# Performance work log

Hardware: AMD Instinct MI355X
Metric: run time of the kernel (lower is better)

## Reference

```python
import jax, jax.numpy as jnp
import numpy as np

BETA = 0.25       # commit-loss weight (beta)
INIT_GAIN = 0.02  # trunc_normal std for codebook init
B, L, D = 4, 4096, 3
VOCAB = 8192


def setup_inputs() -> dict:
    key = jax.random.key(0)
    k1, k2 = jax.random.split(key)
    feats = jax.random.normal(k1, (B, L, D), dtype=jnp.float32)
    # frozen codebook (nn.Embedding weight), trunc_normal(std=0.02) approximated by normal*0.02
    emb = jax.random.normal(k2, (VOCAB, D), dtype=jnp.float32) * INIT_GAIN
    return {"feats": feats, "emb": emb}


def reference(feats, emb):
    b, l, d = feats.shape
    flat = feats.reshape(-1, d)                                # [N, D]
    dist = (jnp.sum(flat * flat, axis=1, keepdims=True)
            - 2.0 * (flat @ emb.T)
            + jnp.sum(emb * emb, axis=1))
    idx = jnp.argmin(dist, axis=1)                             # [N] int
    quant = emb[idx].reshape(b, l, d)                          # gather lookup
    # e_latent_loss: codebook->encoder MSE (feats detached); commit: beta * encoder->codebook MSE
    e_latent_loss = jnp.mean((quant - jax.lax.stop_gradient(feats)) ** 2)
    commit_loss = BETA * jnp.mean((feats - jax.lax.stop_gradient(quant)) ** 2)
    vq_loss = e_latent_loss + commit_loss
    # straight-through estimator
    quant_ste = feats + jax.lax.stop_gradient(quant - feats)
    return quant_ste, idx.reshape(b, l), vq_loss
```

## Files before the change

kernel.cpp:

```cpp
#include <hip/hip_runtime.h>
#include <cstdint>

#define N_ROWS   16384
#define VOCAB    8192
#define CHUNK    1024
#define BLOCK    256
#define NCHUNK   (VOCAB / CHUNK)
#define NRB      (N_ROWS / BLOCK)


__global__ __launch_bounds__(BLOCK) void vq_dist_kernel(
    const float* __restrict__ feats, const float* __restrict__ emb,
    unsigned long long* __restrict__ keys)
{
    __shared__ float4 sE[CHUNK];

    const int chunk = blockIdx.y;
    const int vbase = chunk * CHUNK;

    for (int i = threadIdx.x; i < CHUNK; i += BLOCK) {
        const int v = vbase + i;
        const float e0 = emb[3 * v + 0];
        const float e1 = emb[3 * v + 1];
        const float e2 = emb[3 * v + 2];
        const float ee = __fadd_rn(__fadd_rn(__fmul_rn(e0, e0), __fmul_rn(e1, e1)),
                                   __fmul_rn(e2, e2));
        sE[i] = make_float4(e0, e1, e2, ee);
    }
    __syncthreads();

    const int row = blockIdx.x * BLOCK + threadIdx.x;
    const float x0 = feats[3 * row + 0];
    const float x1 = feats[3 * row + 1];
    const float x2 = feats[3 * row + 2];
    const float xx = __fadd_rn(__fadd_rn(__fmul_rn(x0, x0), __fmul_rn(x1, x1)),
                               __fmul_rn(x2, x2));

    float best = __int_as_float(0x7f800000);
    int   bidx = 0;

    #pragma unroll 8
    for (int i = 0; i < CHUNK; ++i) {
        const float4 E = sE[i];
        const float xe = __fmaf_rn(x2, E.z, __fmaf_rn(x1, E.y, __fmul_rn(x0, E.x)));
        const float d = __fadd_rn(__fsub_rn(xx, __fmul_rn(2.0f, xe)), E.w);
        if (d < best) { best = d; bidx = i; }
    }

    const unsigned long long key =
        ((unsigned long long)__float_as_uint(best) << 32) |
        (unsigned long long)(unsigned)(vbase + bidx);
    atomicMin(&keys[row], key);
}

__global__ __launch_bounds__(BLOCK) void vq_finalize_kernel(
    const float* __restrict__ feats, const float* __restrict__ emb,
    const unsigned long long* __restrict__ keys,
    float* __restrict__ out_quant, float* __restrict__ out_idx,
    float* __restrict__ partial)
{
    const int row = blockIdx.x * BLOCK + threadIdx.x;
    const unsigned long long key = keys[row];
    const unsigned idx = (unsigned)(key & 0xffffffffULL);

    const float x0 = feats[3 * row + 0];
    const float x1 = feats[3 * row + 1];
    const float x2 = feats[3 * row + 2];
    const float e0 = emb[3 * idx + 0];
    const float e1 = emb[3 * idx + 1];
    const float e2 = emb[3 * idx + 2];

    out_quant[3 * row + 0] = __fadd_rn(x0, __fsub_rn(e0, x0));
    out_quant[3 * row + 1] = __fadd_rn(x1, __fsub_rn(e1, x1));
    out_quant[3 * row + 2] = __fadd_rn(x2, __fsub_rn(e2, x2));
    out_idx[row] = (float)idx;

    const float d0 = e0 - x0, d1 = e1 - x1, d2 = e2 - x2;
    float s = d0 * d0 + d1 * d1 + d2 * d2;

    #pragma unroll
    for (int off = 32; off > 0; off >>= 1) s += __shfl_down(s, off, 64);

    __shared__ float wsum[BLOCK / 64];
    if ((threadIdx.x & 63) == 0) wsum[threadIdx.x >> 6] = s;
    __syncthreads();
    if (threadIdx.x == 0)
        partial[blockIdx.x] = (wsum[0] + wsum[1]) + (wsum[2] + wsum[3]);
}

__global__ void vq_loss_kernel(const float* __restrict__ partial,
                               float* __restrict__ out_loss)
{
    float s = partial[threadIdx.x];
    #pragma unroll
    for (int off = 32; off > 0; off >>= 1) s += __shfl_down(s, off, 64);
    if (threadIdx.x == 0) {
        const float m = s / (float)(N_ROWS * 3);
        out_loss[0] = __fadd_rn(m, __fmul_rn(0.25f, m));
    }
}

extern "C" void kernel_launch(void* const* d_in, const int* in_sizes, int n_in,
                              void* d_out, int out_size, void* d_ws, size_t ws_size,
                              hipStream_t stream)
{
    const float* feats = (const float*)d_in[0];
    const float* emb   = (const float*)d_in[1];
    float* out = (float*)d_out;

    unsigned long long* keys = (unsigned long long*)d_ws;
    float* partial = (float*)((char*)d_ws + (size_t)N_ROWS * 8);

    hipMemsetAsync(d_ws, 0xFF, (size_t)N_ROWS * 8, stream);

    vq_dist_kernel<<<dim3(NRB, NCHUNK), BLOCK, 0, stream>>>(feats, emb, keys);
    vq_finalize_kernel<<<NRB, BLOCK, 0, stream>>>(
        feats, emb, keys, out, out + (size_t)N_ROWS * 3, partial);
    vq_loss_kernel<<<1, 64, 0, stream>>>(partial, out + (size_t)N_ROWS * 4);
}
```

Measured before the change: 90.67 us.

## Fuse distance search and finalize into one kernel with 16 lanes per row

Replaces the chunked distance kernel plus 64-bit global atomicMin with one kernel. Each block handles 32 rows, 16 lanes per row, and streams the whole codebook through shared memory in 8 pieces, prefetching the next piece into registers. The row's argmin is reduced with wave shuffles, and the gather, quantized output and loss partial are written in the same kernel, which removes the memset, the atomics and the separate finalize launch. The cost is that every block now reads the full codebook and synchronises 16 times, and only 1 in 16 lanes does the epilogue work.

```diff
diff --git a/kernel.cpp b/kernel.cpp
--- a/kernel.cpp
+++ b/kernel.cpp
@@ -3,99 +3,113 @@
 
 #define N_ROWS   16384
 #define VOCAB    8192
-#define CHUNK    1024
-#define BLOCK    256
-#define NCHUNK   (VOCAB / CHUNK)
-#define NRB      (N_ROWS / BLOCK)
+#define BLOCK    512
+#define ROWS_PB  32
+#define NPIECE   8
+#define PIECE    1024
+#define GRID     (N_ROWS / ROWS_PB)
+
+typedef unsigned long long u64;
 
 
-__global__ __launch_bounds__(BLOCK) void vq_dist_kernel(
+__global__ __launch_bounds__(BLOCK, 4) void vq_main_kernel(
     const float* __restrict__ feats, const float* __restrict__ emb,
-    unsigned long long* __restrict__ keys)
+    float* __restrict__ out_quant, float* __restrict__ out_idx,
+    float* __restrict__ partial)
 {
-    __shared__ float4 sE[CHUNK];
+    __shared__ float4 sE[PIECE];
+    __shared__ float  wsum[BLOCK / 64];
 
-    const int chunk = blockIdx.y;
-    const int vbase = chunk * CHUNK;
+    const int tid = threadIdx.x;
+    const int c   = tid & 15;
+    const int row = blockIdx.x * ROWS_PB + (tid >> 4);
 
-    for (int i = threadIdx.x; i < CHUNK; i += BLOCK) {
-        const int v = vbase + i;
-        const float e0 = emb[3 * v + 0];
-        const float e1 = emb[3 * v + 1];
-        const float e2 = emb[3 * v + 2];
-        const float ee = __fadd_rn(__fadd_rn(__fmul_rn(e0, e0), __fmul_rn(e1, e1)),
-                                   __fmul_rn(e2, e2));
-        sE[i] = make_float4(e0, e1, e2, ee);
-    }
-    __syncthreads();
-
-    const int row = blockIdx.x * BLOCK + threadIdx.x;
     const float x0 = feats[3 * row + 0];
     const float x1 = feats[3 * row + 1];
     const float x2 = feats[3 * row + 2];
     const float xx = __fadd_rn(__fadd_rn(__fmul_rn(x0, x0), __fmul_rn(x1, x1)),
                                __fmul_rn(x2, x2));
 
+    const float* g = emb + 3 * tid;
+    float a0 = g[0],    a1 = g[1],    a2 = g[2];
+    float b0 = g[1536], b1 = g[1537], b2 = g[1538];
+
     float best = __int_as_float(0x7f800000);
-    int   bidx = 0;
+    int   bj   = 0;
 
-    #pragma unroll 8
-    for (int i = 0; i < CHUNK; ++i) {
-        const float4 E = sE[i];
-        const float xe = __fmaf_rn(x2, E.z, __fmaf_rn(x1, E.y, __fmul_rn(x0, E.x)));
-        const float d = __fadd_rn(__fsub_rn(xx, __fmul_rn(2.0f, xe)), E.w);
-        if (d < best) { best = d; bidx = i; }
+    for (int p = 0; p < NPIECE; ++p) {
+        __syncthreads();
+        sE[tid] = make_float4(a0, a1, a2,
+            __fadd_rn(__fadd_rn(__fmul_rn(a0, a0), __fmul_rn(a1, a1)), __fmul_rn(a2, a2)));
+        sE[tid + BLOCK] = make_float4(b0, b1, b2,
+            __fadd_rn(__fadd_rn(__fmul_rn(b0, b0), __fmul_rn(b1, b1)), __fmul_rn(b2, b2)));
+        __syncthreads();
+
+        if (p + 1 < NPIECE) {
+            const float* gn = emb + 3 * ((p + 1) * PIECE + tid);
+            a0 = gn[0];    a1 = gn[1];    a2 = gn[2];
+            b0 = gn[1536]; b1 = gn[1537]; b2 = gn[1538];
+        }
+
+        float pbest = __int_as_float(0x7f800000);
+        int   pj    = 0;
+        #pragma unroll
+        for (int j = 0; j < 64; ++j) {
+            const float4 E = sE[j * 16 + c];
+            const float xe = __fmaf_rn(x2, E.z, __fmaf_rn(x1, E.y, __fmul_rn(x0, E.x)));
+            const float d  = __fadd_rn(__fsub_rn(xx, __fadd_rn(xe, xe)), E.w);
+            if (d < pbest) { pbest = d; pj = j; }
+        }
+        if (pbest < best) { best = pbest; bj = p * 64 + pj; }
     }
 
-    const unsigned long long key =
-        ((unsigned long long)__float_as_uint(best) << 32) |
-        (unsigned long long)(unsigned)(vbase + bidx);
-    atomicMin(&keys[row], key);
+    u64 key = ((u64)__float_as_uint(best) << 32) | (unsigned)(bj * 16 + c);
+    #pragma unroll
+    for (int off = 1; off < 16; off <<= 1) {
+        const u64 other = __shfl_xor(key, off, 64);
+        if (other < key) key = other;
+    }
+
+    float s = 0.0f;
+    if (c == 0) {
+        const unsigned idx = (unsigned)(key & 0xffffffffULL);
+        const float e0 = emb[3 * idx + 0];
+        const float e1 = emb[3 * idx + 1];
+        const float e2 = emb[3 * idx + 2];
+        out_quant[3 * row + 0] = __fadd_rn(x0, __fsub_rn(e0, x0));
+        out_quant[3 * row + 1] = __fadd_rn(x1, __fsub_rn(e1, x1));
+        out_quant[3 * row + 2] = __fadd_rn(x2, __fsub_rn(e2, x2));
+        out_idx[row] = (float)idx;
+        const float d0 = e0 - x0, d1 = e1 - x1, d2 = e2 - x2;
+        s = d0 * d0 + d1 * d1 + d2 * d2;
+    }
+
+    #pragma unroll
+    for (int off = 1; off < 64; off <<= 1) s += __shfl_xor(s, off, 64);
+    if ((tid & 63) == 0) wsum[tid >> 6] = s;
+    __syncthreads();
+    if (tid == 0) {
+        float t = 0.0f;
+        #pragma unroll
+        for (int w = 0; w < BLOCK / 64; ++w) t += wsum[w];
+        partial[blockIdx.x] = t;
+    }
 }
 
-__global__ __launch_bounds__(BLOCK) void vq_finalize_kernel(
-    const float* __restrict__ feats, const float* __restrict__ emb,
-    const unsigned long long* __restrict__ keys,
-    float* __restrict__ out_quant, float* __restrict__ out_idx,
-    float* __restrict__ partial)
+__global__ __launch_bounds__(GRID) void vq_loss_kernel(
+    const float* __restrict__ partial, float* __restrict__ out_loss)
 {
-    const int row = blockIdx.x * BLOCK + threadIdx.x;
-    const unsigned long long key = keys[row];
-    const unsigned idx = (unsigned)(key & 0xffffffffULL);
-
-    const float x0 = feats[3 * row + 0];
-    const float x1 = feats[3 * row + 1];
-    const float x2 = feats[3 * row + 2];
-    const float e0 = emb[3 * idx + 0];
-    const float e1 = emb[3 * idx + 1];
-    const float e2 = emb[3 * idx + 2];
-
-    out_quant[3 * row + 0] = __fadd_rn(x0, __fsub_rn(e0, x0));
-    out_quant[3 * row + 1] = __fadd_rn(x1, __fsub_rn(e1, x1));
-    out_quant[3 * row + 2] = __fadd_rn(x2, __fsub_rn(e2, x2));
-    out_idx[row] = (float)idx;
-
-    const float d0 = e0 - x0, d1 = e1 - x1, d2 = e2 - x2;
-    float s = d0 * d0 + d1 * d1 + d2 * d2;
-
+    __shared__ float wsum[GRID / 64];
+    float s = partial[threadIdx.x];
     #pragma unroll
-    for (int off = 32; off > 0; off >>= 1) s += __shfl_down(s, off, 64);
-
-    __shared__ float wsum[BLOCK / 64];
+    for (int off = 1; off < 64; off <<= 1) s += __shfl_xor(s, off, 64);
     if ((threadIdx.x & 63) == 0) wsum[threadIdx.x >> 6] = s;
     __syncthreads();
-    if (threadIdx.x == 0)
-        partial[blockIdx.x] = (wsum[0] + wsum[1]) + (wsum[2] + wsum[3]);
-}
-
-__global__ void vq_loss_kernel(const float* __restrict__ partial,
-                               float* __restrict__ out_loss)
-{
-    float s = partial[threadIdx.x];
-    #pragma unroll
-    for (int off = 32; off > 0; off >>= 1) s += __shfl_down(s, off, 64);
     if (threadIdx.x == 0) {
-        const float m = s / (float)(N_ROWS * 3);
+        float t = 0.0f;
+        #pragma unroll
+        for (int w = 0; w < GRID / 64; ++w) t += wsum[w];
+        const float m = t / (float)(N_ROWS * 3);
         out_loss[0] = __fadd_rn(m, __fmul_rn(0.25f, m));
     }
 }
@@ -107,14 +121,9 @@
     const float* feats = (const float*)d_in[0];
     const float* emb   = (const float*)d_in[1];
     float* out = (float*)d_out;
+    float* partial = (float*)d_ws;
 
-    unsigned long long* keys = (unsigned long long*)d_ws;
-    float* partial = (float*)((char*)d_ws + (size_t)N_ROWS * 8);
-
-    hipMemsetAsync(d_ws, 0xFF, (size_t)N_ROWS * 8, stream);
-
-    vq_dist_kernel<<<dim3(NRB, NCHUNK), BLOCK, 0, stream>>>(feats, emb, keys);
-    vq_finalize_kernel<<<NRB, BLOCK, 0, stream>>>(
-        feats, emb, keys, out, out + (size_t)N_ROWS * 3, partial);
-    vq_loss_kernel<<<1, 64, 0, stream>>>(partial, out + (size_t)N_ROWS * 4);
+    vq_main_kernel<<<GRID, BLOCK, 0, stream>>>(
+        feats, emb, out, out + (size_t)N_ROWS * 3, partial);
+    vq_loss_kernel<<<1, GRID, 0, stream>>>(partial, out + (size_t)N_ROWS * 4);
 }
```

Result: faster. 83.31 us (-8.1%).
